# Performance work log

Hardware: AMD Instinct MI355X
Metric: run time of the kernel (lower is better)

Reference implementation:

```python
import jax, jax.numpy as jnp
import numpy as np

B, H, W, C = 4, 64, 64, 512
EPS = 1e-3  # keras BatchNormalization default epsilon


def setup_inputs() -> dict:
    key = jax.random.key(0)
    ks = jax.random.split(key, 16)
    c8, c2 = C // 8, C // 2
    sc = lambda fan_in: 1.0 / np.sqrt(fan_in)
    inp = {
        "x": jax.random.normal(ks[0], (B, H, W, C), dtype=jnp.float32),
        # 1x1 conv weights as [Cin, Cout] matrices
        "wf": jax.random.normal(ks[1], (C, c8), dtype=jnp.float32) * sc(C),
        "bf": jnp.zeros((c8,), jnp.float32),
        "wg": jax.random.normal(ks[2], (C, c8), dtype=jnp.float32) * sc(C),
        "bg": jnp.zeros((c8,), jnp.float32),
        "wh": jax.random.normal(ks[3], (C, c2), dtype=jnp.float32) * sc(C),
        "bh": jnp.zeros((c2,), jnp.float32),
        "wo": jax.random.normal(ks[4], (c2, C), dtype=jnp.float32) * sc(c2),
        "bo": jnp.zeros((C,), jnp.float32),
        "gamma": jax.random.normal(ks[5], (1,), dtype=jnp.float32) * 0.05,
        # concat 1x1 conv (2C -> C), has bias (use_batchnorm=False default)
        "wc": jax.random.normal(ks[6], (2 * C, C), dtype=jnp.float32) * sc(2 * C),
        "bc": jnp.zeros((C,), jnp.float32),
        # BN inference params (moving statistics)
        "bn_scale": jnp.ones((C,), jnp.float32),
        "bn_bias": jnp.zeros((C,), jnp.float32),
        "bn_mean": jnp.zeros((C,), jnp.float32),
        "bn_var": jnp.ones((C,), jnp.float32),
    }
    return inp


def reference(x, wf, bf, wg, bg, wh, bh, wo, bo, gamma, wc, bc,
              bn_scale, bn_bias, bn_mean, bn_var):
    b, h, w, c = x.shape
    n = h * w
    xf = x.reshape(b, n, c)
    f = xf @ wf + bf          # [B, N, C/8]
    g = xf @ wg + bg          # [B, N, C/8]
    hv = xf @ wh + bh         # [B, N, C/2]
    s = jnp.einsum('bnd,bmd->bnm', g, f)   # [B, N, N]
    beta = jax.nn.softmax(s, axis=-1)
    o = jnp.einsum('bnm,bmd->bnd', beta, hv)  # [B, N, C/2]
    o = o @ wo + bo                            # [B, N, C]
    att = gamma * o + xf                       # gamma-scaled residual
    cat = jnp.concatenate([att, xf], axis=-1)  # [B, N, 2C]
    y = cat @ wc + bc
    # BatchNorm inference + relu
    y = (y - bn_mean) * (bn_scale / jnp.sqrt(bn_var + EPS)) + bn_bias
    y = jax.nn.relu(y)
    return y.reshape(b, h, w, c)
```

## Files before the change

kernel.cpp:

```cpp
#include <hip/hip_runtime.h>
#include <hip/hip_bf16.h>

typedef __bf16 bf16x8 __attribute__((ext_vector_type(8)));
typedef float f32x4 __attribute__((ext_vector_type(4)));

#define EPSBN 1e-3f

constexpr int NPIX = 4096;
constexpr int D2 = 256;

#define RAW_BARRIER() do { \
  asm volatile("s_waitcnt lgkmcnt(0)" ::: "memory"); \
  __builtin_amdgcn_s_barrier(); \
  asm volatile("" ::: "memory"); \
} while (0)

__global__ __launch_bounds__(256) void k_cvt(const float* __restrict__ x,
                                             __bf16* __restrict__ xb, int n4) {
  int i = blockIdx.x * 256 + threadIdx.x;
  if (i >= n4) return;
  float4 v = reinterpret_cast<const float4*>(x)[i];
  union { __bf16 h[4]; uint2 u; } o;
  o.h[0] = (__bf16)v.x; o.h[1] = (__bf16)v.y; o.h[2] = (__bf16)v.z; o.h[3] = (__bf16)v.w;
  reinterpret_cast<uint2*>(xb)[i] = o.u;
}

__global__ __launch_bounds__(256) void kp_wfgh(const float* __restrict__ wf,
                                               const float* __restrict__ wg,
                                               const float* __restrict__ wh,
                                               __bf16* __restrict__ WT) {
  int idx = blockIdx.x * 256 + threadIdx.x;
  int c = idx >> 9, k = idx & 511;
  float v = (c < 64) ? wf[k * 64 + c] : (c < 128) ? wg[k * 64 + (c - 64)] : wh[k * 256 + (c - 128)];
  WT[idx] = (__bf16)v;
}

__global__ __launch_bounds__(128) void kp_bias384(const float* bf_, const float* bg_,
                                                  const float* bh_, float* bias) {
  int c = blockIdx.x * 128 + threadIdx.x;
  bias[c] = (c < 64) ? bf_[c] : (c < 128) ? bg_[c - 64] : bh_[c - 128];
}

__global__ __launch_bounds__(256) void kp_wow(const float* __restrict__ wo,
                                              const float* __restrict__ wc,
                                              float* __restrict__ Wow) {
  int idx = blockIdx.x * 256 + threadIdx.x;
  int d = idx >> 9, c = idx & 511;
  float a0 = 0.f, a1 = 0.f, a2 = 0.f, a3 = 0.f;
  for (int j = 0; j < 512; j += 4) {
    float4 w4 = *reinterpret_cast<const float4*>(wo + d * 512 + j);
    a0 += w4.x * wc[(size_t)j * 512 + c];
    a1 += w4.y * wc[(size_t)(j + 1) * 512 + c];
    a2 += w4.z * wc[(size_t)(j + 2) * 512 + c];
    a3 += w4.w * wc[(size_t)(j + 3) * 512 + c];
  }
  Wow[idx] = (a0 + a1) + (a2 + a3);
}

__global__ __launch_bounds__(256) void kp_wcat(const float* __restrict__ Wow,
                                               const float* __restrict__ wc,
                                               const float* __restrict__ gamma,
                                               const float* __restrict__ bns,
                                               const float* __restrict__ bnv,
                                               __bf16* __restrict__ WT) {
  int idx = blockIdx.x * 256 + threadIdx.x;
  int c = idx / 768, k = idx % 768;
  float s = bns[c] * rsqrtf(bnv[c] + EPSBN);
  float v;
  if (k < 256) v = gamma[0] * Wow[k * 512 + c] * s;
  else { int kk = k - 256; v = (wc[kk * 512 + c] + wc[(512 + kk) * 512 + c]) * s; }
  WT[idx] = (__bf16)v;
}

__global__ __launch_bounds__(256) void kp_biasF(const float* bo, const float* wc, const float* bc,
                                                const float* gamma, const float* bns, const float* bnb,
                                                const float* bnm, const float* bnv, float* biasF) {
  int c = blockIdx.x * 256 + threadIdx.x;
  float s = bns[c] * rsqrtf(bnv[c] + EPSBN);
  float a0 = 0.f, a1 = 0.f, a2 = 0.f, a3 = 0.f;
  for (int j = 0; j < 512; j += 4) {
    a0 += bo[j] * wc[(size_t)j * 512 + c];
    a1 += bo[j + 1] * wc[(size_t)(j + 1) * 512 + c];
    a2 += bo[j + 2] * wc[(size_t)(j + 2) * 512 + c];
    a3 += bo[j + 3] * wc[(size_t)(j + 3) * 512 + c];
  }
  float pre = bc[c] + gamma[0] * ((a0 + a1) + (a2 + a3));
  biasF[c] = (pre - bnm[c]) * s + bnb[c];
}

template <int KT, int NC, int MODE>
__global__ __launch_bounds__(256) void k_gemm(const __bf16* __restrict__ A1, int k1, int lda1,
                                              const __bf16* __restrict__ A2, int lda2,
                                              const __bf16* __restrict__ WT,
                                              const float* __restrict__ bias,
                                              void* __restrict__ out1,
                                              void* __restrict__ out2) {
  __shared__ __bf16 As[128][72];
  __shared__ __bf16 Ws[64][72];
  const int m0 = blockIdx.x * 128, n0 = blockIdx.y * 64;
  const int tid = threadIdx.x, lane = tid & 63, w = tid >> 6;
  const int wr = w >> 1, wcl = w & 1;
  const int l15 = lane & 15, l4 = lane >> 4;
  f32x4 acc[4][2] = {};
  for (int ks = 0; ks < KT; ks += 64) {
    const __bf16* Asrc; int lda, kb;
    if (ks < k1) { Asrc = A1; lda = lda1; kb = ks; }
    else         { Asrc = A2; lda = lda2; kb = ks - k1; }
#pragma unroll
    for (int it = 0; it < 4; ++it) {
      int idx = it * 256 + tid, r = idx >> 3, ch = idx & 7;
      *(bf16x8*)(&As[r][ch * 8]) = *(const bf16x8*)(Asrc + (size_t)(m0 + r) * lda + kb + ch * 8);
    }
#pragma unroll
    for (int it = 0; it < 2; ++it) {
      int idx = it * 256 + tid, r = idx >> 3, ch = idx & 7;
      *(bf16x8*)(&Ws[r][ch * 8]) = *(const bf16x8*)(WT + (size_t)(n0 + r) * KT + ks + ch * 8);
    }
    __syncthreads();
#pragma unroll
    for (int kk = 0; kk < 2; ++kk) {
      int krd = kk * 32 + l4 * 8;
      bf16x8 av[4], bv[2];
#pragma unroll
      for (int mi = 0; mi < 4; ++mi) av[mi] = *(const bf16x8*)(&As[wr * 64 + mi * 16 + l15][krd]);
#pragma unroll
      for (int ni = 0; ni < 2; ++ni) bv[ni] = *(const bf16x8*)(&Ws[wcl * 32 + ni * 16 + l15][krd]);
#pragma unroll
      for (int mi = 0; mi < 4; ++mi)
#pragma unroll
        for (int ni = 0; ni < 2; ++ni)
          acc[mi][ni] = __builtin_amdgcn_mfma_f32_16x16x32_bf16(av[mi], bv[ni], acc[mi][ni], 0, 0, 0);
    }
    __syncthreads();
  }
  if (MODE == 1) {
#pragma unroll
    for (int mi = 0; mi < 4; ++mi)
#pragma unroll
      for (int ni = 0; ni < 2; ++ni) {
        int col = n0 + wcl * 32 + ni * 16 + l15;
        float bcol = bias[col];
        int row0 = m0 + wr * 64 + mi * 16 + l4 * 4;
        float* out = (float*)out1;
#pragma unroll
        for (int r = 0; r < 4; ++r)
          out[(size_t)(row0 + r) * NC + col] = fmaxf(acc[mi][ni][r] + bcol, 0.f);
      }
  } else if (n0 < 128) {
#pragma unroll
    for (int mi = 0; mi < 4; ++mi)
#pragma unroll
      for (int ni = 0; ni < 2; ++ni) {
        int col = n0 + wcl * 32 + ni * 16 + l15;
        float bcol = bias[col];
        int row0 = m0 + wr * 64 + mi * 16 + l4 * 4;
        __bf16* fg = (__bf16*)out1;
#pragma unroll
        for (int r = 0; r < 4; ++r)
          fg[(size_t)(row0 + r) * 128 + col] = (__bf16)(acc[mi][ni][r] + bcol);
      }
  } else {
    __syncthreads();
    __bf16 (*Tt)[136] = (__bf16(*)[136])(&As[0][0]);
#pragma unroll
    for (int mi = 0; mi < 4; ++mi)
#pragma unroll
      for (int ni = 0; ni < 2; ++ni) {
        int dloc = wcl * 32 + ni * 16 + l15;
        float bcol = bias[n0 + dloc];
        int nloc = wr * 64 + mi * 16 + l4 * 4;
#pragma unroll
        for (int r = 0; r < 4; ++r)
          Tt[dloc][nloc + r] = (__bf16)(acc[mi][ni][r] + bcol);
      }
    __syncthreads();
    const int bb = m0 >> 12, n = m0 & 4095, d0 = n0 - 128;
    __bf16* hvT = (__bf16*)out2;
    const int rrow = tid >> 3, c8 = tid & 7;
#pragma unroll
    for (int rep = 0; rep < 2; ++rep) {
      int dl = rrow + rep * 32;
      __bf16* dst = hvT + ((size_t)(bb * 256 + d0 + dl)) * 4096 + n;
      *(bf16x8*)(dst + c8 * 8) = *(const bf16x8*)(&Tt[dl][c8 * 8]);
      *(bf16x8*)(dst + 64 + c8 * 8) = *(const bf16x8*)(&Tt[dl][64 + c8 * 8]);
    }
  }
}

__global__ __launch_bounds__(512, 2) void k_attn(const __bf16* __restrict__ fg,
                                                 const __bf16* __restrict__ hvT,
                                                 __bf16* __restrict__ obuf) {
  __shared__ __bf16 PsT[2][64][136];
  __shared__ float Lp[8][64];
  const int id = blockIdx.x;
  const int xcd = id & 7, i2 = id >> 3;
  const int b = xcd >> 1;
  const int q0 = (i2 * 2 + (xcd & 1)) * 64;
  const int tid = threadIdx.x, w = tid >> 6, lane = tid & 63;
  const int l15 = lane & 15, l4 = lane >> 4;
  const __bf16* fgb = fg + (size_t)b * NPIX * 128;
  const __bf16* vb = hvT + (size_t)b * D2 * NPIX;

  bf16x8 bG[4][2];
#pragma unroll
  for (int qt = 0; qt < 4; ++qt)
#pragma unroll
    for (int kk = 0; kk < 2; ++kk)
      bG[qt][kk] = *(const bf16x8*)(fgb + (size_t)(q0 + qt * 16 + l15) * 128 + 64 + kk * 32 + l4 * 8);

  bf16x8 aF[2], bVA[2][4], bVB[2][4];
#pragma unroll
  for (int kk = 0; kk < 2; ++kk)
    aF[kk] = *(const bf16x8*)(fgb + (size_t)(w * 16 + l15) * 128 + kk * 32 + l4 * 8);
#pragma unroll
  for (int dj = 0; dj < 2; ++dj)
#pragma unroll
    for (int k4 = 0; k4 < 4; ++k4) {
      bVA[dj][k4] = *(const bf16x8*)(vb + (size_t)(w * 32 + dj * 16 + l15) * NPIX + k4 * 32 + l4 * 8);
      bVB[dj][k4] = *(const bf16x8*)(vb + (size_t)(w * 32 + dj * 16 + l15) * NPIX + 128 + k4 * 32 + l4 * 8);
    }

  f32x4 accO[4][2] = {};
  float lsum[4] = {0.f, 0.f, 0.f, 0.f};

#define ABODY(T, BV) do {                                                               \
    const int mn1 = (((T) + 1) * 128) & (NPIX - 1);                                     \
    const int mn2 = (((T) + 2) * 128) & (NPIX - 1);                                     \
    const int bufi = (T) & 1;                                                           \
    f32x4 s[4];                                                                         \
    _Pragma("unroll")                                                                   \
    for (int qt = 0; qt < 4; ++qt) {                                                    \
      s[qt] = (f32x4){0.f, 0.f, 0.f, 0.f};                                              \
      _Pragma("unroll")                                                                 \
      for (int kk = 0; kk < 2; ++kk)                                                    \
        s[qt] = __builtin_amdgcn_mfma_f32_16x16x32_bf16(aF[kk], bG[qt][kk], s[qt], 0, 0, 0); \
    }                                                                                   \
    bf16x8 aFn[2];                                                                      \
    _Pragma("unroll")                                                                   \
    for (int kk = 0; kk < 2; ++kk)                                                      \
      aFn[kk] = *(const bf16x8*)(fgb + (size_t)(mn1 + w * 16 + l15) * 128 + kk * 32 + l4 * 8); \
    _Pragma("unroll")                                                                   \
    for (int qt = 0; qt < 4; ++qt) {                                                    \
      float p0 = __expf(s[qt][0]), p1 = __expf(s[qt][1]);                               \
      float p2 = __expf(s[qt][2]), p3 = __expf(s[qt][3]);                               \
      lsum[qt] += (p0 + p1) + (p2 + p3);                                                \
      union { __bf16 h[4]; uint2 u; } pk;                                               \
      pk.h[0] = (__bf16)p0; pk.h[1] = (__bf16)p1;                                       \
      pk.h[2] = (__bf16)p2; pk.h[3] = (__bf16)p3;                                       \
      *(uint2*)(&PsT[bufi][qt * 16 + l15][w * 16 + l4 * 4]) = pk.u;                     \
    }                                                                                   \
    RAW_BARRIER();                                                                      \
    _Pragma("unroll")                                                                   \
    for (int qt = 0; qt < 4; ++qt) {                                                    \
      bf16x8 aP[4];                                                                     \
      _Pragma("unroll")                                                                 \
      for (int k4 = 0; k4 < 4; ++k4)                                                    \
        aP[k4] = *(const bf16x8*)(&PsT[bufi][qt * 16 + l15][k4 * 32 + l4 * 8]);         \
      _Pragma("unroll")                                                                 \
      for (int dj = 0; dj < 2; ++dj)                                                    \
        _Pragma("unroll")                                                               \
        for (int k4 = 0; k4 < 4; ++k4)                                                  \
          accO[qt][dj] = __builtin_amdgcn_mfma_f32_16x16x32_bf16(aP[k4], BV[dj][k4], accO[qt][dj], 0, 0, 0); \
    }                                                                                   \
    _Pragma("unroll")                                                                   \
    for (int dj = 0; dj < 2; ++dj)                                                      \
      _Pragma("unroll")                                                                 \
      for (int k4 = 0; k4 < 4; ++k4)                                                    \
        BV[dj][k4] = *(const bf16x8*)(vb + (size_t)(w * 32 + dj * 16 + l15) * NPIX + mn2 + k4 * 32 + l4 * 8); \
    aF[0] = aFn[0]; aF[1] = aFn[1];                                                     \
  } while (0)

  for (int t = 0; t < 32; t += 2) {
    ABODY(t, bVA);
    ABODY(t + 1, bVB);
  }
#undef ABODY

#pragma unroll
  for (int qt = 0; qt < 4; ++qt) {
    float v = lsum[qt];
    v += __shfl_xor(v, 16); v += __shfl_xor(v, 32);
    lsum[qt] = v;
  }
  if (l4 == 0) {
#pragma unroll
    for (int qt = 0; qt < 4; ++qt) Lp[w][qt * 16 + l15] = lsum[qt];
  }
  __syncthreads();
  float inv[4][4];
#pragma unroll
  for (int qt = 0; qt < 4; ++qt)
#pragma unroll
    for (int r = 0; r < 4; ++r) {
      int q = qt * 16 + l4 * 4 + r;
      float lt = 0.f;
#pragma unroll
      for (int ww = 0; ww < 8; ++ww) lt += Lp[ww][q];
      inv[qt][r] = 1.0f / lt;
    }
  __bf16* ob = obuf + ((size_t)b * NPIX + q0) * D2;
#pragma unroll
  for (int qt = 0; qt < 4; ++qt)
#pragma unroll
    for (int dj = 0; dj < 2; ++dj)
#pragma unroll
      for (int r = 0; r < 4; ++r)
        ob[(size_t)(qt * 16 + l4 * 4 + r) * D2 + w * 32 + dj * 16 + l15] =
            (__bf16)(accO[qt][dj][r] * inv[qt][r]);
}

extern "C" void kernel_launch(void* const* d_in, const int* in_sizes, int n_in,
                              void* d_out, int out_size, void* d_ws, size_t ws_size,
                              hipStream_t stream) {
  const float* x = (const float*)d_in[0];
  const float* wf = (const float*)d_in[1];
  const float* bf_ = (const float*)d_in[2];
  const float* wg = (const float*)d_in[3];
  const float* bg_ = (const float*)d_in[4];
  const float* wh = (const float*)d_in[5];
  const float* bh_ = (const float*)d_in[6];
  const float* wo = (const float*)d_in[7];
  const float* bo = (const float*)d_in[8];
  const float* gamma = (const float*)d_in[9];
  const float* wc = (const float*)d_in[10];
  const float* bc = (const float*)d_in[11];
  const float* bns = (const float*)d_in[12];
  const float* bnb = (const float*)d_in[13];
  const float* bnm = (const float*)d_in[14];
  const float* bnv = (const float*)d_in[15];
  (void)in_sizes; (void)n_in; (void)out_size; (void)ws_size;

  char* ws = (char*)d_ws;
  __bf16* xb     = (__bf16*)(ws + 0);
  __bf16* fg     = (__bf16*)(ws + 16777216);
  __bf16* hvT    = (__bf16*)(ws + 20971520);
  __bf16* obuf   = (__bf16*)(ws + 29360128);
  __bf16* WfghT  = (__bf16*)(ws + 37748736);
  float*  bias384= (float*) (ws + 38141952);
  float*  Wow    = (float*) (ws + 38143488);
  __bf16* WcatT  = (__bf16*)(ws + 38667776);
  float*  biasF  = (float*) (ws + 39454208);
  float* out = (float*)d_out;

  hipLaunchKernelGGL(k_cvt, dim3(8192), dim3(256), 0, stream, x, xb, 2097152);
  hipLaunchKernelGGL(kp_wfgh, dim3(768), dim3(256), 0, stream, wf, wg, wh, WfghT);
  hipLaunchKernelGGL(kp_bias384, dim3(3), dim3(128), 0, stream, bf_, bg_, bh_, bias384);
  hipLaunchKernelGGL(kp_wow, dim3(512), dim3(256), 0, stream, wo, wc, Wow);
  hipLaunchKernelGGL(kp_wcat, dim3(1536), dim3(256), 0, stream, Wow, wc, gamma, bns, bnv, WcatT);
  hipLaunchKernelGGL(kp_biasF, dim3(2), dim3(256), 0, stream, bo, wc, bc, gamma, bns, bnb, bnm, bnv, biasF);
  hipLaunchKernelGGL((k_gemm<512, 384, 0>), dim3(128, 6), dim3(256), 0, stream,
                     xb, 512, 512, xb, 512, WfghT, bias384, (void*)fg, (void*)hvT);
  hipLaunchKernelGGL(k_attn, dim3(256), dim3(512), 0, stream, fg, hvT, obuf);
  hipLaunchKernelGGL((k_gemm<768, 512, 1>), dim3(128, 8), dim3(256), 0, stream,
                     obuf, 256, 256, xb, 512, WcatT, biasF, (void*)out, nullptr);
}
```

Measured before the change: 269.7 us.

## Fuse prep kernels into one launch and widen GEMM tiles to 128x128

```diff
diff --git a/kernel.cpp b/kernel.cpp
--- a/kernel.cpp
+++ b/kernel.cpp
@@ -15,77 +15,74 @@
   asm volatile("" ::: "memory"); \
 } while (0)
 
-__global__ __launch_bounds__(256) void k_cvt(const float* __restrict__ x,
-                                             __bf16* __restrict__ xb, int n4) {
-  int i = blockIdx.x * 256 + threadIdx.x;
-  if (i >= n4) return;
-  float4 v = reinterpret_cast<const float4*>(x)[i];
-  union { __bf16 h[4]; uint2 u; } o;
-  o.h[0] = (__bf16)v.x; o.h[1] = (__bf16)v.y; o.h[2] = (__bf16)v.z; o.h[3] = (__bf16)v.w;
-  reinterpret_cast<uint2*>(xb)[i] = o.u;
-}
-
-__global__ __launch_bounds__(256) void kp_wfgh(const float* __restrict__ wf,
+__global__ __launch_bounds__(256) void kp_prep(const float* __restrict__ x,
+                                               const float* __restrict__ wf,
                                                const float* __restrict__ wg,
                                                const float* __restrict__ wh,
-                                               __bf16* __restrict__ WT) {
-  int idx = blockIdx.x * 256 + threadIdx.x;
-  int c = idx >> 9, k = idx & 511;
-  float v = (c < 64) ? wf[k * 64 + c] : (c < 128) ? wg[k * 64 + (c - 64)] : wh[k * 256 + (c - 128)];
-  WT[idx] = (__bf16)v;
-}
-
-__global__ __launch_bounds__(128) void kp_bias384(const float* bf_, const float* bg_,
-                                                  const float* bh_, float* bias) {
-  int c = blockIdx.x * 128 + threadIdx.x;
-  bias[c] = (c < 64) ? bf_[c] : (c < 128) ? bg_[c - 64] : bh_[c - 128];
-}
-
-__global__ __launch_bounds__(256) void kp_wow(const float* __restrict__ wo,
-                                              const float* __restrict__ wc,
-                                              float* __restrict__ Wow) {
-  int idx = blockIdx.x * 256 + threadIdx.x;
-  int d = idx >> 9, c = idx & 511;
-  float a0 = 0.f, a1 = 0.f, a2 = 0.f, a3 = 0.f;
-  for (int j = 0; j < 512; j += 4) {
-    float4 w4 = *reinterpret_cast<const float4*>(wo + d * 512 + j);
-    a0 += w4.x * wc[(size_t)j * 512 + c];
-    a1 += w4.y * wc[(size_t)(j + 1) * 512 + c];
-    a2 += w4.z * wc[(size_t)(j + 2) * 512 + c];
-    a3 += w4.w * wc[(size_t)(j + 3) * 512 + c];
-  }
-  Wow[idx] = (a0 + a1) + (a2 + a3);
-}
-
-__global__ __launch_bounds__(256) void kp_wcat(const float* __restrict__ Wow,
+                                               const float* __restrict__ bf_,
+                                               const float* __restrict__ bg_,
+                                               const float* __restrict__ bh_,
+                                               const float* __restrict__ wo,
+                                               const float* __restrict__ bo,
+                                               const float* __restrict__ gamma,
                                                const float* __restrict__ wc,
-                                               const float* __restrict__ gamma,
+                                               const float* __restrict__ bc,
                                                const float* __restrict__ bns,
+                                               const float* __restrict__ bnb,
+                                               const float* __restrict__ bnm,
                                                const float* __restrict__ bnv,
-                                               __bf16* __restrict__ WT) {
-  int idx = blockIdx.x * 256 + threadIdx.x;
-  int c = idx / 768, k = idx % 768;
-  float s = bns[c] * rsqrtf(bnv[c] + EPSBN);
-  float v;
-  if (k < 256) v = gamma[0] * Wow[k * 512 + c] * s;
-  else { int kk = k - 256; v = (wc[kk * 512 + c] + wc[(512 + kk) * 512 + c]) * s; }
-  WT[idx] = (__bf16)v;
-}
-
-__global__ __launch_bounds__(256) void kp_biasF(const float* bo, const float* wc, const float* bc,
-                                                const float* gamma, const float* bns, const float* bnb,
-                                                const float* bnm, const float* bnv, float* biasF) {
-  int c = blockIdx.x * 256 + threadIdx.x;
-  float s = bns[c] * rsqrtf(bnv[c] + EPSBN);
-  float a0 = 0.f, a1 = 0.f, a2 = 0.f, a3 = 0.f;
-  for (int j = 0; j < 512; j += 4) {
-    a0 += bo[j] * wc[(size_t)j * 512 + c];
-    a1 += bo[j + 1] * wc[(size_t)(j + 1) * 512 + c];
-    a2 += bo[j + 2] * wc[(size_t)(j + 2) * 512 + c];
-    a3 += bo[j + 3] * wc[(size_t)(j + 3) * 512 + c];
-  }
-  float pre = bc[c] + gamma[0] * ((a0 + a1) + (a2 + a3));
-  biasF[c] = (pre - bnm[c]) * s + bnb[c];
+                                               __bf16* __restrict__ xb,
+                                               __bf16* __restrict__ WfghT,
+                                               float* __restrict__ bias384,
+                                               __bf16* __restrict__ WcatT,
+                                               float* __restrict__ biasF) {
+  const int bid = blockIdx.x, tid = threadIdx.x;
+  if (bid < 768) {
+    int idx = bid * 256 + tid;
+    int c = idx >> 9, k = idx & 511;
+    float v = (c < 64) ? wf[k * 64 + c] : (c < 128) ? wg[k * 64 + (c - 64)] : wh[k * 256 + (c - 128)];
+    WfghT[idx] = (__bf16)v;
+  } else if (bid < 770) {
+    int c = (bid - 768) * 256 + tid;
+    if (c < 384) bias384[c] = (c < 64) ? bf_[c] : (c < 128) ? bg_[c - 64] : bh_[c - 128];
+  } else if (bid < 8962) {
+    int i = (bid - 770) * 256 + tid;
+    float4 v = reinterpret_cast<const float4*>(x)[i];
+    union { __bf16 h[4]; uint2 u; } o;
+    o.h[0] = (__bf16)v.x; o.h[1] = (__bf16)v.y; o.h[2] = (__bf16)v.z; o.h[3] = (__bf16)v.w;
+    reinterpret_cast<uint2*>(xb)[i] = o.u;
+  } else if (bid < 9474) {
+    int idx = (bid - 8962) * 256 + tid;
+    int d = idx >> 9, c = idx & 511;
+    float a0 = 0.f, a1 = 0.f, a2 = 0.f, a3 = 0.f;
+    for (int j = 0; j < 512; j += 4) {
+      float4 w4 = *reinterpret_cast<const float4*>(wo + d * 512 + j);
+      a0 += w4.x * wc[(size_t)j * 512 + c];
+      a1 += w4.y * wc[(size_t)(j + 1) * 512 + c];
+      a2 += w4.z * wc[(size_t)(j + 2) * 512 + c];
+      a3 += w4.w * wc[(size_t)(j + 3) * 512 + c];
+    }
+    float s = bns[c] * rsqrtf(bnv[c] + EPSBN);
+    WcatT[(size_t)c * 768 + d] = (__bf16)(gamma[0] * ((a0 + a1) + (a2 + a3)) * s);
+  } else if (bid < 10498) {
+    int idx = (bid - 9474) * 256 + tid;
+    int c = idx >> 9, kk = idx & 511;
+    float s = bns[c] * rsqrtf(bnv[c] + EPSBN);
+    float v = (wc[(size_t)kk * 512 + c] + wc[(size_t)(512 + kk) * 512 + c]) * s;
+    WcatT[(size_t)c * 768 + 256 + kk] = (__bf16)v;
+  } else {
+    int c = (bid - 10498) * 256 + tid;
+    float s = bns[c] * rsqrtf(bnv[c] + EPSBN);
+    float a0 = 0.f, a1 = 0.f, a2 = 0.f, a3 = 0.f;
+    for (int j = 0; j < 512; j += 4) {
+      a0 += bo[j] * wc[(size_t)j * 512 + c];
+      a1 += bo[j + 1] * wc[(size_t)(j + 1) * 512 + c];
+      a2 += bo[j + 2] * wc[(size_t)(j + 2) * 512 + c];
+      a3 += bo[j + 3] * wc[(size_t)(j + 3) * 512 + c];
+    }
+    float pre = bc[c] + gamma[0] * ((a0 + a1) + (a2 + a3));
+    biasF[c] = (pre - bnm[c]) * s + bnb[c];
+  }
 }
 
 template <int KT, int NC, int MODE>
@@ -95,13 +92,12 @@
                                               const float* __restrict__ bias,
                                               void* __restrict__ out1,
                                               void* __restrict__ out2) {
-  __shared__ __bf16 As[128][72];
-  __shared__ __bf16 Ws[64][72];
-  const int m0 = blockIdx.x * 128, n0 = blockIdx.y * 64;
+  __shared__ __bf16 SH[256][72];
+  const int m0 = blockIdx.x * 128, n0 = blockIdx.y * 128;
   const int tid = threadIdx.x, lane = tid & 63, w = tid >> 6;
   const int wr = w >> 1, wcl = w & 1;
   const int l15 = lane & 15, l4 = lane >> 4;
-  f32x4 acc[4][2] = {};
+  f32x4 acc[4][4] = {};
   for (int ks = 0; ks < KT; ks += 64) {
     const __bf16* Asrc; int lda, kb;
     if (ks < k1) { Asrc = A1; lda = lda1; kb = ks; }
@@ -109,64 +105,64 @@
 #pragma unroll
     for (int it = 0; it < 4; ++it) {
       int idx = it * 256 + tid, r = idx >> 3, ch = idx & 7;
-      *(bf16x8*)(&As[r][ch * 8]) = *(const bf16x8*)(Asrc + (size_t)(m0 + r) * lda + kb + ch * 8);
-    }
-#pragma unroll
-    for (int it = 0; it < 2; ++it) {
+      *(bf16x8*)(&SH[r][ch * 8]) = *(const bf16x8*)(Asrc + (size_t)(m0 + r) * lda + kb + ch * 8);
+    }
+#pragma unroll
+    for (int it = 0; it < 4; ++it) {
       int idx = it * 256 + tid, r = idx >> 3, ch = idx & 7;
-      *(bf16x8*)(&Ws[r][ch * 8]) = *(const bf16x8*)(WT + (size_t)(n0 + r) * KT + ks + ch * 8);
+      *(bf16x8*)(&SH[128 + r][ch * 8]) = *(const bf16x8*)(WT + (size_t)(n0 + r) * KT + ks + ch * 8);
     }
     __syncthreads();
 #pragma unroll
     for (int kk = 0; kk < 2; ++kk) {
       int krd = kk * 32 + l4 * 8;
-      bf16x8 av[4], bv[2];
-#pragma unroll
-      for (int mi = 0; mi < 4; ++mi) av[mi] = *(const bf16x8*)(&As[wr * 64 + mi * 16 + l15][krd]);
-#pragma unroll
-      for (int ni = 0; ni < 2; ++ni) bv[ni] = *(const bf16x8*)(&Ws[wcl * 32 + ni * 16 + l15][krd]);
+      bf16x8 av[4], bv[4];
+#pragma unroll
+      for (int mi = 0; mi < 4; ++mi) av[mi] = *(const bf16x8*)(&SH[wr * 64 + mi * 16 + l15][krd]);
+#pragma unroll
+      for (int ni = 0; ni < 4; ++ni) bv[ni] = *(const bf16x8*)(&SH[128 + wcl * 64 + ni * 16 + l15][krd]);
 #pragma unroll
       for (int mi = 0; mi < 4; ++mi)
 #pragma unroll
-        for (int ni = 0; ni < 2; ++ni)
+        for (int ni = 0; ni < 4; ++ni)
           acc[mi][ni] = __builtin_amdgcn_mfma_f32_16x16x32_bf16(av[mi], bv[ni], acc[mi][ni], 0, 0, 0);
     }
     __syncthreads();
   }
   if (MODE == 1) {
+    float* out = (float*)out1;
 #pragma unroll
     for (int mi = 0; mi < 4; ++mi)
 #pragma unroll
-      for (int ni = 0; ni < 2; ++ni) {
-        int col = n0 + wcl * 32 + ni * 16 + l15;
+      for (int ni = 0; ni < 4; ++ni) {
+        int col = n0 + wcl * 64 + ni * 16 + l15;
         float bcol = bias[col];
         int row0 = m0 + wr * 64 + mi * 16 + l4 * 4;
-        float* out = (float*)out1;
 #pragma unroll
         for (int r = 0; r < 4; ++r)
           out[(size_t)(row0 + r) * NC + col] = fmaxf(acc[mi][ni][r] + bcol, 0.f);
       }
-  } else if (n0 < 128) {
+  } else if (n0 == 0) {
+    __bf16* fg = (__bf16*)out1;
 #pragma unroll
     for (int mi = 0; mi < 4; ++mi)
 #pragma unroll
-      for (int ni = 0; ni < 2; ++ni) {
-        int col = n0 + wcl * 32 + ni * 16 + l15;
+      for (int ni = 0; ni < 4; ++ni) {
+        int col = wcl * 64 + ni * 16 + l15;
         float bcol = bias[col];
         int row0 = m0 + wr * 64 + mi * 16 + l4 * 4;
-        __bf16* fg = (__bf16*)out1;
 #pragma unroll
         for (int r = 0; r < 4; ++r)
           fg[(size_t)(row0 + r) * 128 + col] = (__bf16)(acc[mi][ni][r] + bcol);
       }
   } else {
     __syncthreads();
-    __bf16 (*Tt)[136] = (__bf16(*)[136])(&As[0][0]);
+    __bf16 (*Tt)[136] = (__bf16(*)[136])(&SH[0][0]);
 #pragma unroll
     for (int mi = 0; mi < 4; ++mi)
 #pragma unroll
-      for (int ni = 0; ni < 2; ++ni) {
-        int dloc = wcl * 32 + ni * 16 + l15;
+      for (int ni = 0; ni < 4; ++ni) {
+        int dloc = wcl * 64 + ni * 16 + l15;
         float bcol = bias[n0 + dloc];
         int nloc = wr * 64 + mi * 16 + l4 * 4;
 #pragma unroll
@@ -176,14 +172,11 @@
     __syncthreads();
     const int bb = m0 >> 12, n = m0 & 4095, d0 = n0 - 128;
     __bf16* hvT = (__bf16*)out2;
-    const int rrow = tid >> 3, c8 = tid & 7;
-#pragma unroll
-    for (int rep = 0; rep < 2; ++rep) {
-      int dl = rrow + rep * 32;
-      __bf16* dst = hvT + ((size_t)(bb * 256 + d0 + dl)) * 4096 + n;
-      *(bf16x8*)(dst + c8 * 8) = *(const bf16x8*)(&Tt[dl][c8 * 8]);
-      *(bf16x8*)(dst + 64 + c8 * 8) = *(const bf16x8*)(&Tt[dl][64 + c8 * 8]);
-    }
+    const int rrow = tid >> 1, c8 = tid & 1;
+    __bf16* dst = hvT + ((size_t)(bb * 256 + d0 + rrow)) * 4096 + n;
+#pragma unroll
+    for (int j = 0; j < 8; ++j)
+      *(bf16x8*)(dst + c8 * 64 + j * 8) = *(const bf16x8*)(&Tt[rrow][c8 * 64 + j * 8]);
   }
 }
 
@@ -337,20 +330,16 @@
   __bf16* obuf   = (__bf16*)(ws + 29360128);
   __bf16* WfghT  = (__bf16*)(ws + 37748736);
   float*  bias384= (float*) (ws + 38141952);
-  float*  Wow    = (float*) (ws + 38143488);
-  __bf16* WcatT  = (__bf16*)(ws + 38667776);
-  float*  biasF  = (float*) (ws + 39454208);
+  __bf16* WcatT  = (__bf16*)(ws + 38143488);
+  float*  biasF  = (float*) (ws + 38929920);
   float* out = (float*)d_out;
 
-  hipLaunchKernelGGL(k_cvt, dim3(8192), dim3(256), 0, stream, x, xb, 2097152);
-  hipLaunchKernelGGL(kp_wfgh, dim3(768), dim3(256), 0, stream, wf, wg, wh, WfghT);
-  hipLaunchKernelGGL(kp_bias384, dim3(3), dim3(128), 0, stream, bf_, bg_, bh_, bias384);
-  hipLaunchKernelGGL(kp_wow, dim3(512), dim3(256), 0, stream, wo, wc, Wow);
-  hipLaunchKernelGGL(kp_wcat, dim3(1536), dim3(256), 0, stream, Wow, wc, gamma, bns, bnv, WcatT);
-  hipLaunchKernelGGL(kp_biasF, dim3(2), dim3(256), 0, stream, bo, wc, bc, gamma, bns, bnb, bnm, bnv, biasF);
-  hipLaunchKernelGGL((k_gemm<512, 384, 0>), dim3(128, 6), dim3(256), 0, stream,
+  hipLaunchKernelGGL(kp_prep, dim3(10500), dim3(256), 0, stream,
+                     x, wf, wg, wh, bf_, bg_, bh_, wo, bo, gamma, wc, bc,
+                     bns, bnb, bnm, bnv, xb, WfghT, bias384, WcatT, biasF);
+  hipLaunchKernelGGL((k_gemm<512, 384, 0>), dim3(128, 3), dim3(256), 0, stream,
                      xb, 512, 512, xb, 512, WfghT, bias384, (void*)fg, (void*)hvT);
   hipLaunchKernelGGL(k_attn, dim3(256), dim3(512), 0, stream, fg, hvT, obuf);
-  hipLaunchKernelGGL((k_gemm<768, 512, 1>), dim3(128, 8), dim3(256), 0, stream,
+  hipLaunchKernelGGL((k_gemm<768, 512, 1>), dim3(128, 4), dim3(256), 0, stream,
                      obuf, 256, 256, xb, 512, WcatT, biasF, (void*)out, nullptr);
 }
```

Result: no change. 272.1 us (+0.9%).
